# Optimization experiments

Hardware: AMD Instinct MI355X
Metric: run time of the kernel (lower is better)

The kernel has to match this reference:

```python
import jax, jax.numpy as jnp
import numpy as np

B, LQ, LK = 8, 256, 256
Q_SIZE = K_SIZE = H = D_V = 256
MASK_VALUE = -1000000.0


def setup_inputs() -> dict:
    key = jax.random.key(0)
    kq, kk, kv, kl, kwq, kwk, kwv = jax.random.split(key, 7)
    # Linear weights, torch nn.Linear stores (out, in); init ~ U(-1/sqrt(in), 1/sqrt(in))
    def lin(k, out_f, in_f):
        bound = 1.0 / np.sqrt(in_f)
        return jax.random.uniform(k, (out_f, in_f), jnp.float32, -bound, bound)
    return {
        "queries": jax.random.normal(kq, (B, LQ, Q_SIZE), jnp.float32),
        "keyes": jax.random.normal(kk, (B, LK, K_SIZE), jnp.float32),
        "values": jax.random.normal(kv, (B, LK, D_V), jnp.float32),
        "valid_lens": jax.random.randint(kl, (B,), 1, LK + 1),
        "W_q": lin(kwq, H, Q_SIZE),
        "W_k": lin(kwk, H, K_SIZE),
        "W_v": lin(kwv, 1, H),
    }


def reference(queries, keyes, values, valid_lens, W_q, W_k, W_v):
    # Projections (nn.Linear without bias): x @ W.T
    q = jnp.einsum("bqd,hd->bqh", queries, W_q)            # (B, Lq, H)
    k = jnp.einsum("bkd,hd->bkh", keyes, W_k)              # (B, Lk, H)
    # Broadcast-add + tanh: (B, Lq, Lk, H)
    features = jnp.tanh(q[:, :, None, :] + k[:, None, :, :])
    # W_v reduction H -> 1, squeeze: scores (B, Lq, Lk)
    scores = jnp.einsum("bqkh,h->bqk", features, W_v[0])
    # sequence_mask over the last (key) axis with value -1e6
    lk = scores.shape[-1]
    mask = jnp.arange(lk)[None, None, :] < valid_lens[:, None, None]  # (B,1,Lk)
    scores = jnp.where(mask, scores, MASK_VALUE)
    # NOTE: this repo's masked_softmax normalizes over dim=1 (the query axis),
    # faithfully reproduced here.
    attention_weights = jax.nn.softmax(scores, axis=1)
    # dropout is identity in eval / p=0.0
    return jnp.einsum("bqk,bkd->bqd", attention_weights, values)
```

## Files before the change

### kernel.cpp

```cpp
#include <hip/hip_runtime.h>

typedef float vf4 __attribute__((ext_vector_type(4)));

#define MASKV (-1000000.0f)
#define LOG2E 1.4426950408889634f
#define TWO_LOG2E 2.8853900817779268f

__device__ __forceinline__ float fexp2(float x) {
#if __has_builtin(__builtin_amdgcn_exp2f)
  return __builtin_amdgcn_exp2f(x);
#else
  return exp2f(x);
#endif
}
__device__ __forceinline__ float frcp(float x) {
#if __has_builtin(__builtin_amdgcn_rcpf)
  return __builtin_amdgcn_rcpf(x);
#else
  return 1.0f / x;
#endif
}

__global__ __launch_bounds__(256) void proj_kernel(
    const float* __restrict__ queries, const float* __restrict__ keyes,
    const float* __restrict__ Wq, const float* __restrict__ Wk,
    float* __restrict__ Qp, float* __restrict__ Kp) {
  __shared__ alignas(16) float At[16 * 68];
  __shared__ alignas(16) float Bt[16 * 68];
  const int t = threadIdx.x;
  const int m0 = blockIdx.x * 64;
  const int n0 = blockIdx.y * 64;
  const bool isQ = (m0 < 2048);
  const float* X = isQ ? queries : keyes;
  const float* W = isQ ? Wq : Wk;
  float* C = isQ ? Qp : Kp;
  const int mb = isQ ? m0 : (m0 - 2048);

  const int lm = t >> 2;
  const int lq = t & 3;
  const int mm4 = (t & 15) * 4;
  const int nn4 = (t >> 4) * 4;

  float acc[4][4] = {};
  for (int kc = 0; kc < 256; kc += 16) {
    __syncthreads();
    vf4 xa = *(const vf4*)&X[(mb + lm) * 256 + kc + lq * 4];
    vf4 wb = *(const vf4*)&W[(n0 + lm) * 256 + kc + lq * 4];
#pragma unroll
    for (int c = 0; c < 4; ++c) {
      At[(lq * 4 + c) * 68 + lm] = xa[c];
      Bt[(lq * 4 + c) * 68 + lm] = wb[c];
    }
    __syncthreads();
#pragma unroll
    for (int kk = 0; kk < 16; ++kk) {
      vf4 a4 = *(const vf4*)&At[kk * 68 + mm4];
      vf4 b4 = *(const vf4*)&Bt[kk * 68 + nn4];
#pragma unroll
      for (int i = 0; i < 4; ++i)
#pragma unroll
        for (int j = 0; j < 4; ++j) acc[i][j] += a4[i] * b4[j];
    }
  }
#pragma unroll
  for (int i = 0; i < 4; ++i) {
    vf4 o = {acc[i][0] * TWO_LOG2E, acc[i][1] * TWO_LOG2E,
             acc[i][2] * TWO_LOG2E, acc[i][3] * TWO_LOG2E};
    *(vf4*)&C[(mb + mm4 + i) * 256 + n0 + nn4] = o;
  }
}

__global__ __launch_bounds__(256) void scores_kernel(
    const float* __restrict__ Qp, const float* __restrict__ Kp,
    const float* __restrict__ Wv, const int* __restrict__ valid_lens,
    float* __restrict__ ST) {
  __shared__ alignas(16) float Qc[32 * 36];
  __shared__ alignas(16) float Kc[32 * 36];
  __shared__ alignas(16) float wvs[256];
  const int t = threadIdx.x;
  const int b = blockIdx.z;
  const int i0 = blockIdx.x * 32;
  const int j0 = blockIdx.y * 32;

  if (t < 64) *(vf4*)&wvs[t * 4] = *(const vf4*)&Wv[t * 4];
  __syncthreads();

  float Swv;
  {
    vf4 w4 = *(const vf4*)&wvs[(t & 63) * 4];
    float sw = w4[0] + w4[1] + w4[2] + w4[3];
#pragma unroll
    for (int off = 1; off < 64; off <<= 1) sw += __shfl_xor(sw, off, 64);
    Swv = sw;
  }

  const int lr = t >> 3, lq = t & 7;
  const int ti = t & 15, tj = t >> 4;
  float acc[2][2] = {};

  for (int hc = 0; hc < 8; ++hc) {
    __syncthreads();
    vf4 qv = *(const vf4*)&Qp[((b << 8) + i0 + lr) * 256 + hc * 32 + lq * 4];
    vf4 kv = *(const vf4*)&Kp[((b << 8) + j0 + lr) * 256 + hc * 32 + lq * 4];
    *(vf4*)&Qc[lr * 36 + lq * 4] = qv;
    *(vf4*)&Kc[lr * 36 + lq * 4] = kv;
    __syncthreads();
#pragma unroll
    for (int hh = 0; hh < 8; ++hh) {
      vf4 q0 = *(const vf4*)&Qc[ti * 36 + hh * 4];
      vf4 q1 = *(const vf4*)&Qc[(ti + 16) * 36 + hh * 4];
      vf4 k0 = *(const vf4*)&Kc[tj * 36 + hh * 4];
      vf4 k1 = *(const vf4*)&Kc[(tj + 16) * 36 + hh * 4];
      vf4 wv4 = *(const vf4*)&wvs[hc * 32 + hh * 4];
#pragma unroll
      for (int c = 0; c < 4; ++c) {
        acc[0][0] += wv4[c] * frcp(fexp2(q0[c] + k0[c]) + 1.0f);
        acc[0][1] += wv4[c] * frcp(fexp2(q0[c] + k1[c]) + 1.0f);
        acc[1][0] += wv4[c] * frcp(fexp2(q1[c] + k0[c]) + 1.0f);
        acc[1][1] += wv4[c] * frcp(fexp2(q1[c] + k1[c]) + 1.0f);
      }
    }
  }
  const int len = valid_lens[b];
#pragma unroll
  for (int jq = 0; jq < 2; ++jq) {
    const int jg = j0 + tj + jq * 16;
    const bool masked = (jg >= len);
#pragma unroll
    for (int iq = 0; iq < 2; ++iq) {
      const int ig = i0 + ti + iq * 16;
      float s = masked ? MASKV : (Swv - 2.0f * acc[iq][jq]);
      ST[(((b << 8) + jg) << 8) + ig] = s;
    }
  }
}

__global__ __launch_bounds__(256) void softmax_kernel(float* __restrict__ ST) {
  const int t = threadIdx.x;
  const int l = t & 63;
  const int row = blockIdx.x * 4 + (t >> 6);
  vf4* rp = (vf4*)(ST + row * 256);
  vf4 v = rp[l];
  float mx = fmaxf(fmaxf(v[0], v[1]), fmaxf(v[2], v[3]));
#pragma unroll
  for (int off = 1; off < 64; off <<= 1) mx = fmaxf(mx, __shfl_xor(mx, off, 64));
  vf4 e;
#pragma unroll
  for (int c = 0; c < 4; ++c) e[c] = fexp2((v[c] - mx) * LOG2E);
  float s = e[0] + e[1] + e[2] + e[3];
#pragma unroll
  for (int off = 1; off < 64; off <<= 1) s += __shfl_xor(s, off, 64);
  const float r = frcp(s);
#pragma unroll
  for (int c = 0; c < 4; ++c) e[c] *= r;
  rp[l] = e;
}

__global__ __launch_bounds__(256) void out_kernel(
    const float* __restrict__ WT, const float* __restrict__ V,
    float* __restrict__ out) {
  __shared__ alignas(16) float Ws[32 * 36];
  __shared__ alignas(16) float Vs[32 * 36];
  const int t = threadIdx.x;
  const int b = blockIdx.z;
  const int i0 = blockIdx.x * 32;
  const int d0 = blockIdx.y * 32;
  const int jj = t >> 3, lq = t & 7;
  const int ii = t >> 3, dd = (t & 7) * 4;
  vf4 acc = {0.f, 0.f, 0.f, 0.f};
  for (int jc = 0; jc < 8; ++jc) {
    __syncthreads();
    const int jg = jc * 32 + jj;
    *(vf4*)&Ws[jj * 36 + lq * 4] = *(const vf4*)&WT[((b << 8) + jg) * 256 + i0 + lq * 4];
    *(vf4*)&Vs[jj * 36 + lq * 4] = *(const vf4*)&V[((b << 8) + jg) * 256 + d0 + lq * 4];
    __syncthreads();
#pragma unroll
    for (int j2 = 0; j2 < 32; ++j2) {
      const float w = Ws[j2 * 36 + ii];
      vf4 v4 = *(const vf4*)&Vs[j2 * 36 + dd];
      acc += w * v4;
    }
  }
  *(vf4*)&out[((b << 8) + i0 + ii) * 256 + d0 + dd] = acc;
}

extern "C" void kernel_launch(void* const* d_in, const int* in_sizes, int n_in,
                              void* d_out, int out_size, void* d_ws, size_t ws_size,
                              hipStream_t stream) {
  const float* queries = (const float*)d_in[0];
  const float* keyes = (const float*)d_in[1];
  const float* values = (const float*)d_in[2];
  const int* valid_lens = (const int*)d_in[3];
  const float* Wq = (const float*)d_in[4];
  const float* Wk = (const float*)d_in[5];
  const float* Wv = (const float*)d_in[6];
  float* out = (float*)d_out;

  float* Qp = (float*)d_ws;
  float* Kp = Qp + 524288;
  float* ST = Kp + 524288;

  proj_kernel<<<dim3(64, 4, 1), 256, 0, stream>>>(queries, keyes, Wq, Wk, Qp, Kp);
  scores_kernel<<<dim3(8, 8, 8), 256, 0, stream>>>(Qp, Kp, Wv, valid_lens, ST);
  softmax_kernel<<<512, 256, 0, stream>>>(ST);
  out_kernel<<<dim3(8, 8, 8), 256, 0, stream>>>(ST, values, out);
}
```

Baseline: 126.9 us.

## Fuse softmax into scores kernel and retile output GEMM

The scores kernel now has each block compute all 256 query rows for 8 key columns, so the softmax over the query axis runs in registers via wave shuffles before the weights are written. This removes the separate softmax kernel and one read-write pass over the score matrix. The grid shrinks from 512 to 256 blocks, and each block stages a 256x33 Q tile in shared memory, which may reduce occupancy and latency hiding for the tanh-heavy inner loop. The output GEMM is retiled to 128 threads computing 4x4 register tiles over 32x64 output blocks.

```diff
diff --git a/kernel.cpp b/kernel.cpp
--- a/kernel.cpp
+++ b/kernel.cpp
@@ -6,20 +6,8 @@
 #define LOG2E 1.4426950408889634f
 #define TWO_LOG2E 2.8853900817779268f
 
-__device__ __forceinline__ float fexp2(float x) {
-#if __has_builtin(__builtin_amdgcn_exp2f)
-  return __builtin_amdgcn_exp2f(x);
-#else
-  return exp2f(x);
-#endif
-}
-__device__ __forceinline__ float frcp(float x) {
-#if __has_builtin(__builtin_amdgcn_rcpf)
-  return __builtin_amdgcn_rcpf(x);
-#else
-  return 1.0f / x;
-#endif
-}
+__device__ __forceinline__ float fexp2(float x) { return __builtin_amdgcn_exp2f(x); }
+__device__ __forceinline__ float frcp(float x) { return __builtin_amdgcn_rcpf(x); }
 
 __global__ __launch_bounds__(256) void proj_kernel(
     const float* __restrict__ queries, const float* __restrict__ keyes,
@@ -70,118 +58,148 @@
   }
 }
 
-__global__ __launch_bounds__(256) void scores_kernel(
+__global__ __launch_bounds__(256) void scores_softmax_kernel(
     const float* __restrict__ Qp, const float* __restrict__ Kp,
     const float* __restrict__ Wv, const int* __restrict__ valid_lens,
-    float* __restrict__ ST) {
-  __shared__ alignas(16) float Qc[32 * 36];
-  __shared__ alignas(16) float Kc[32 * 36];
+    float* __restrict__ WT) {
+  __shared__ float Qs[256 * 33 + 8];
+  __shared__ float Ks[8 * 33];
   __shared__ alignas(16) float wvs[256];
+  const int t = threadIdx.x;
+  const int b = blockIdx.y;
+  const int j0 = blockIdx.x * 8;
+  const int ti = t & 63;
+  const int tj = t >> 6;
+
+  if (t < 64) *(vf4*)&wvs[t * 4] = *(const vf4*)&Wv[t * 4];
+  __syncthreads();
+
+  float Swv;
+  {
+    vf4 w4 = *(const vf4*)&wvs[ti * 4];
+    float sw = w4[0] + w4[1] + w4[2] + w4[3];
+#pragma unroll
+    for (int off = 1; off < 64; off <<= 1) sw += __shfl_xor(sw, off, 64);
+    Swv = sw;
+  }
+
+  float acc0[4] = {0.f, 0.f, 0.f, 0.f};
+  float acc1[4] = {0.f, 0.f, 0.f, 0.f};
+  const int qr = t >> 2;
+  const int qc = (t & 3) * 8;
+
+  for (int hc = 0; hc < 8; ++hc) {
+    __syncthreads();
+#pragma unroll
+    for (int s = 0; s < 4; ++s) {
+      const int i = s * 64 + qr;
+      const float* src = &Qp[((b << 8) + i) * 256 + hc * 32 + qc];
+      vf4 a = *(const vf4*)src;
+      vf4 bb = *(const vf4*)(src + 4);
+      float* q = &Qs[i * 33 + qc];
+      q[0] = a[0]; q[1] = a[1]; q[2] = a[2]; q[3] = a[3];
+      q[4] = bb[0]; q[5] = bb[1]; q[6] = bb[2]; q[7] = bb[3];
+    }
+    if (t < 64) {
+      const int jj = t >> 3, c = (t & 7) * 4;
+      vf4 kv = *(const vf4*)&Kp[((b << 8) + j0 + jj) * 256 + hc * 32 + c];
+      float* kd = &Ks[jj * 33 + c];
+      kd[0] = kv[0]; kd[1] = kv[1]; kd[2] = kv[2]; kd[3] = kv[3];
+    }
+    __syncthreads();
+#pragma unroll
+    for (int hh = 0; hh < 8; ++hh) {
+      vf4 wv4 = *(const vf4*)&wvs[hc * 32 + hh * 4];
+      float k0[4], k1[4];
+#pragma unroll
+      for (int c = 0; c < 4; ++c) {
+        k0[c] = Ks[(tj * 2 + 0) * 33 + hh * 4 + c];
+        k1[c] = Ks[(tj * 2 + 1) * 33 + hh * 4 + c];
+      }
+#pragma unroll
+      for (int r = 0; r < 4; ++r) {
+        const float* qp = &Qs[(ti + 64 * r) * 33 + hh * 4];
+#pragma unroll
+        for (int c = 0; c < 4; ++c) {
+          const float qv = qp[c];
+          acc0[r] += wv4[c] * frcp(fexp2(qv + k0[c]) + 1.0f);
+          acc1[r] += wv4[c] * frcp(fexp2(qv + k1[c]) + 1.0f);
+        }
+      }
+    }
+  }
+
+  const int len = valid_lens[b];
+#pragma unroll
+  for (int jj = 0; jj < 2; ++jj) {
+    const int j = j0 + tj * 2 + jj;
+    const bool masked = (j >= len);
+    float sc[4];
+#pragma unroll
+    for (int r = 0; r < 4; ++r) {
+      const float a = (jj == 0) ? acc0[r] : acc1[r];
+      sc[r] = masked ? MASKV : (Swv - 2.0f * a);
+    }
+    float m = fmaxf(fmaxf(sc[0], sc[1]), fmaxf(sc[2], sc[3]));
+#pragma unroll
+    for (int off = 1; off < 64; off <<= 1) m = fmaxf(m, __shfl_xor(m, off, 64));
+    float e[4], es = 0.f;
+#pragma unroll
+    for (int r = 0; r < 4; ++r) { e[r] = fexp2((sc[r] - m) * LOG2E); es += e[r]; }
+#pragma unroll
+    for (int off = 1; off < 64; off <<= 1) es += __shfl_xor(es, off, 64);
+    const float rr = frcp(es);
+    float* dst = &WT[((b << 8) + j) << 8];
+#pragma unroll
+    for (int r = 0; r < 4; ++r) dst[ti + 64 * r] = e[r] * rr;
+  }
+}
+
+__global__ __launch_bounds__(128) void out_kernel(
+    const float* __restrict__ WT, const float* __restrict__ V,
+    float* __restrict__ out) {
+  __shared__ alignas(16) float As[32 * 36];
+  __shared__ alignas(16) float Bs[32 * 68];
   const int t = threadIdx.x;
   const int b = blockIdx.z;
   const int i0 = blockIdx.x * 32;
-  const int j0 = blockIdx.y * 32;
-
-  if (t < 64) *(vf4*)&wvs[t * 4] = *(const vf4*)&Wv[t * 4];
-  __syncthreads();
-
-  float Swv;
-  {
-    vf4 w4 = *(const vf4*)&wvs[(t & 63) * 4];
-    float sw = w4[0] + w4[1] + w4[2] + w4[3];
-#pragma unroll
-    for (int off = 1; off < 64; off <<= 1) sw += __shfl_xor(sw, off, 64);
-    Swv = sw;
-  }
-
-  const int lr = t >> 3, lq = t & 7;
-  const int ti = t & 15, tj = t >> 4;
-  float acc[2][2] = {};
-
-  for (int hc = 0; hc < 8; ++hc) {
-    __syncthreads();
-    vf4 qv = *(const vf4*)&Qp[((b << 8) + i0 + lr) * 256 + hc * 32 + lq * 4];
-    vf4 kv = *(const vf4*)&Kp[((b << 8) + j0 + lr) * 256 + hc * 32 + lq * 4];
-    *(vf4*)&Qc[lr * 36 + lq * 4] = qv;
-    *(vf4*)&Kc[lr * 36 + lq * 4] = kv;
-    __syncthreads();
-#pragma unroll
-    for (int hh = 0; hh < 8; ++hh) {
-      vf4 q0 = *(const vf4*)&Qc[ti * 36 + hh * 4];
-      vf4 q1 = *(const vf4*)&Qc[(ti + 16) * 36 + hh * 4];
-      vf4 k0 = *(const vf4*)&Kc[tj * 36 + hh * 4];
-      vf4 k1 = *(const vf4*)&Kc[(tj + 16) * 36 + hh * 4];
-      vf4 wv4 = *(const vf4*)&wvs[hc * 32 + hh * 4];
-#pragma unroll
-      for (int c = 0; c < 4; ++c) {
-        acc[0][0] += wv4[c] * frcp(fexp2(q0[c] + k0[c]) + 1.0f);
-        acc[0][1] += wv4[c] * frcp(fexp2(q0[c] + k1[c]) + 1.0f);
-        acc[1][0] += wv4[c] * frcp(fexp2(q1[c] + k0[c]) + 1.0f);
-        acc[1][1] += wv4[c] * frcp(fexp2(q1[c] + k1[c]) + 1.0f);
-      }
-    }
-  }
-  const int len = valid_lens[b];
-#pragma unroll
-  for (int jq = 0; jq < 2; ++jq) {
-    const int jg = j0 + tj + jq * 16;
-    const bool masked = (jg >= len);
-#pragma unroll
-    for (int iq = 0; iq < 2; ++iq) {
-      const int ig = i0 + ti + iq * 16;
-      float s = masked ? MASKV : (Swv - 2.0f * acc[iq][jq]);
-      ST[(((b << 8) + jg) << 8) + ig] = s;
-    }
-  }
-}
-
-__global__ __launch_bounds__(256) void softmax_kernel(float* __restrict__ ST) {
-  const int t = threadIdx.x;
-  const int l = t & 63;
-  const int row = blockIdx.x * 4 + (t >> 6);
-  vf4* rp = (vf4*)(ST + row * 256);
-  vf4 v = rp[l];
-  float mx = fmaxf(fmaxf(v[0], v[1]), fmaxf(v[2], v[3]));
-#pragma unroll
-  for (int off = 1; off < 64; off <<= 1) mx = fmaxf(mx, __shfl_xor(mx, off, 64));
-  vf4 e;
-#pragma unroll
-  for (int c = 0; c < 4; ++c) e[c] = fexp2((v[c] - mx) * LOG2E);
-  float s = e[0] + e[1] + e[2] + e[3];
-#pragma unroll
-  for (int off = 1; off < 64; off <<= 1) s += __shfl_xor(s, off, 64);
-  const float r = frcp(s);
-#pragma unroll
-  for (int c = 0; c < 4; ++c) e[c] *= r;
-  rp[l] = e;
-}
-
-__global__ __launch_bounds__(256) void out_kernel(
-    const float* __restrict__ WT, const float* __restrict__ V,
-    float* __restrict__ out) {
-  __shared__ alignas(16) float Ws[32 * 36];
-  __shared__ alignas(16) float Vs[32 * 36];
-  const int t = threadIdx.x;
-  const int b = blockIdx.z;
-  const int i0 = blockIdx.x * 32;
-  const int d0 = blockIdx.y * 32;
-  const int jj = t >> 3, lq = t & 7;
-  const int ii = t >> 3, dd = (t & 7) * 4;
-  vf4 acc = {0.f, 0.f, 0.f, 0.f};
+  const int d0 = blockIdx.y * 64;
+  const int tm = t & 7;
+  const int tn = t >> 3;
+  const int sr = t >> 2;
+  const int sc4 = (t & 3) * 4;
+  float acc[4][4] = {};
   for (int jc = 0; jc < 8; ++jc) {
     __syncthreads();
-    const int jg = jc * 32 + jj;
-    *(vf4*)&Ws[jj * 36 + lq * 4] = *(const vf4*)&WT[((b << 8) + jg) * 256 + i0 + lq * 4];
-    *(vf4*)&Vs[jj * 36 + lq * 4] = *(const vf4*)&V[((b << 8) + jg) * 256 + d0 + lq * 4];
-    __syncthreads();
-#pragma unroll
-    for (int j2 = 0; j2 < 32; ++j2) {
-      const float w = Ws[j2 * 36 + ii];
-      vf4 v4 = *(const vf4*)&Vs[j2 * 36 + dd];
-      acc += w * v4;
-    }
-  }
-  *(vf4*)&out[((b << 8) + i0 + ii) * 256 + d0 + dd] = acc;
+    const int jbase = jc * 32;
+#pragma unroll
+    for (int s = 0; s < 2; ++s) {
+      const int col = sc4 + s * 16;
+      *(vf4*)&As[sr * 36 + col] =
+          *(const vf4*)&WT[((b << 8) + jbase + sr) * 256 + i0 + col];
+    }
+#pragma unroll
+    for (int s = 0; s < 4; ++s) {
+      const int col = sc4 + s * 16;
+      *(vf4*)&Bs[sr * 68 + col] =
+          *(const vf4*)&V[((b << 8) + jbase + sr) * 256 + d0 + col];
+    }
+    __syncthreads();
+#pragma unroll
+    for (int kk = 0; kk < 32; ++kk) {
+      vf4 a4 = *(const vf4*)&As[kk * 36 + tm * 4];
+      vf4 b4 = *(const vf4*)&Bs[kk * 68 + tn * 4];
+#pragma unroll
+      for (int i = 0; i < 4; ++i)
+#pragma unroll
+        for (int j = 0; j < 4; ++j) acc[i][j] += a4[i] * b4[j];
+    }
+  }
+#pragma unroll
+  for (int i = 0; i < 4; ++i) {
+    vf4 o = {acc[i][0], acc[i][1], acc[i][2], acc[i][3]};
+    *(vf4*)&out[((b << 8) + i0 + tm * 4 + i) * 256 + d0 + tn * 4] = o;
+  }
 }
 
 extern "C" void kernel_launch(void* const* d_in, const int* in_sizes, int n_in,
@@ -198,10 +216,9 @@
 
   float* Qp = (float*)d_ws;
   float* Kp = Qp + 524288;
-  float* ST = Kp + 524288;
-
-  proj_kernel<<<dim3(64, 4, 1), 256, 0, stream>>>(queries, keyes, Wq, Wk, Qp, Kp);
-  scores_kernel<<<dim3(8, 8, 8), 256, 0, stream>>>(Qp, Kp, Wv, valid_lens, ST);
-  softmax_kernel<<<512, 256, 0, stream>>>(ST);
-  out_kernel<<<dim3(8, 8, 8), 256, 0, stream>>>(ST, values, out);
-}
+  float* WT = Kp + 524288;
+
+  proj_kernel<<<dim3(64, 4), 256, 0, stream>>>(queries, keyes, Wq, Wk, Qp, Kp);
+  scores_softmax_kernel<<<dim3(32, 8), 256, 0, stream>>>(Qp, Kp, Wv, valid_lens, WT);
+  out_kernel<<<dim3(8, 4, 8), 128, 0, stream>>>(WT, values, out);
+}
```

After: 136.5 us. 7.6% more time.

## Fold softmax exp into scores kernel and apply normalization inside output GEMM

Applied to the files above, without the earlier changes.

The scores kernel now writes exp(score) directly, with no max subtraction, since the scores are bounded by the sum of |W_v|. Masked keys get 1.0, which still gives a uniform softmax across the query axis. A light rowsum kernel stores reciprocal sums, and the output GEMM scales E by them as it loads tiles. This removes the separate softmax read-modify-write pass. The scores kernel also gets an XOR-swizzled LDS layout, and the output kernel is retiled to 4x4 per thread with 128-thread blocks. The risk is that skipping max subtraction could overflow exp if score magnitudes were larger than W_v bounds them to.

```diff
diff --git a/kernel.cpp b/kernel.cpp
--- a/kernel.cpp
+++ b/kernel.cpp
@@ -2,24 +2,11 @@
 
 typedef float vf4 __attribute__((ext_vector_type(4)));
 
-#define MASKV (-1000000.0f)
 #define LOG2E 1.4426950408889634f
 #define TWO_LOG2E 2.8853900817779268f
 
-__device__ __forceinline__ float fexp2(float x) {
-#if __has_builtin(__builtin_amdgcn_exp2f)
-  return __builtin_amdgcn_exp2f(x);
-#else
-  return exp2f(x);
-#endif
-}
-__device__ __forceinline__ float frcp(float x) {
-#if __has_builtin(__builtin_amdgcn_rcpf)
-  return __builtin_amdgcn_rcpf(x);
-#else
-  return 1.0f / x;
-#endif
-}
+__device__ __forceinline__ float fexp2(float x) { return __builtin_amdgcn_exp2f(x); }
+__device__ __forceinline__ float frcp(float x) { return __builtin_amdgcn_rcpf(x); }
 
 __global__ __launch_bounds__(256) void proj_kernel(
     const float* __restrict__ queries, const float* __restrict__ keyes,
@@ -70,118 +57,136 @@
   }
 }
 
-__global__ __launch_bounds__(256) void scores_kernel(
+__global__ __launch_bounds__(256) void scores_exp_kernel(
     const float* __restrict__ Qp, const float* __restrict__ Kp,
     const float* __restrict__ Wv, const int* __restrict__ valid_lens,
-    float* __restrict__ ST) {
-  __shared__ alignas(16) float Qc[32 * 36];
-  __shared__ alignas(16) float Kc[32 * 36];
+    float* __restrict__ E) {
+  __shared__ alignas(16) float Qs[32 * 32];
+  __shared__ alignas(16) float Ks[32 * 32];
   __shared__ alignas(16) float wvs[256];
   const int t = threadIdx.x;
-  const int b = blockIdx.z;
   const int i0 = blockIdx.x * 32;
   const int j0 = blockIdx.y * 32;
-
-  if (t < 64) *(vf4*)&wvs[t * 4] = *(const vf4*)&Wv[t * 4];
-  __syncthreads();
+  const int b = blockIdx.z;
+  const int ti = t & 15;
+  const int tj = t >> 4;
 
   float Swv;
   {
-    vf4 w4 = *(const vf4*)&wvs[(t & 63) * 4];
+    vf4 w4 = *(const vf4*)&Wv[(t & 63) * 4];
     float sw = w4[0] + w4[1] + w4[2] + w4[3];
 #pragma unroll
     for (int off = 1; off < 64; off <<= 1) sw += __shfl_xor(sw, off, 64);
     Swv = sw;
   }
-
-  const int lr = t >> 3, lq = t & 7;
-  const int ti = t & 15, tj = t >> 4;
+  if (t < 64) *(vf4*)&wvs[t * 4] = *(const vf4*)&Wv[t * 4];
+
+  const int srow = t >> 3;
+  const int scg = t & 7;
+  const int swcol = ((scg ^ (srow & 7)) << 2);
+  const int qxor = ti & 7;
+  const int kxor = tj & 7;
+
   float acc[2][2] = {};
-
   for (int hc = 0; hc < 8; ++hc) {
     __syncthreads();
-    vf4 qv = *(const vf4*)&Qp[((b << 8) + i0 + lr) * 256 + hc * 32 + lq * 4];
-    vf4 kv = *(const vf4*)&Kp[((b << 8) + j0 + lr) * 256 + hc * 32 + lq * 4];
-    *(vf4*)&Qc[lr * 36 + lq * 4] = qv;
-    *(vf4*)&Kc[lr * 36 + lq * 4] = kv;
+    vf4 qv = *(const vf4*)&Qp[(((b << 8) + i0 + srow) << 8) + hc * 32 + scg * 4];
+    vf4 kv = *(const vf4*)&Kp[(((b << 8) + j0 + srow) << 8) + hc * 32 + scg * 4];
+    *(vf4*)&Qs[srow * 32 + swcol] = qv;
+    *(vf4*)&Ks[srow * 32 + swcol] = kv;
     __syncthreads();
 #pragma unroll
     for (int hh = 0; hh < 8; ++hh) {
-      vf4 q0 = *(const vf4*)&Qc[ti * 36 + hh * 4];
-      vf4 q1 = *(const vf4*)&Qc[(ti + 16) * 36 + hh * 4];
-      vf4 k0 = *(const vf4*)&Kc[tj * 36 + hh * 4];
-      vf4 k1 = *(const vf4*)&Kc[(tj + 16) * 36 + hh * 4];
+      vf4 q0 = *(const vf4*)&Qs[ti * 32 + ((hh ^ qxor) << 2)];
+      vf4 q1 = *(const vf4*)&Qs[(ti + 16) * 32 + ((hh ^ qxor) << 2)];
+      vf4 k0 = *(const vf4*)&Ks[tj * 32 + ((hh ^ kxor) << 2)];
+      vf4 k1 = *(const vf4*)&Ks[(tj + 16) * 32 + ((hh ^ kxor) << 2)];
       vf4 wv4 = *(const vf4*)&wvs[hc * 32 + hh * 4];
 #pragma unroll
-      for (int c = 0; c < 4; ++c) {
-        acc[0][0] += wv4[c] * frcp(fexp2(q0[c] + k0[c]) + 1.0f);
-        acc[0][1] += wv4[c] * frcp(fexp2(q0[c] + k1[c]) + 1.0f);
-        acc[1][0] += wv4[c] * frcp(fexp2(q1[c] + k0[c]) + 1.0f);
-        acc[1][1] += wv4[c] * frcp(fexp2(q1[c] + k1[c]) + 1.0f);
+      for (int e = 0; e < 4; ++e) {
+        const float we = wv4[e];
+        acc[0][0] += we * frcp(fexp2(q0[e] + k0[e]) + 1.0f);
+        acc[0][1] += we * frcp(fexp2(q0[e] + k1[e]) + 1.0f);
+        acc[1][0] += we * frcp(fexp2(q1[e] + k0[e]) + 1.0f);
+        acc[1][1] += we * frcp(fexp2(q1[e] + k1[e]) + 1.0f);
       }
     }
   }
+
   const int len = valid_lens[b];
 #pragma unroll
-  for (int jq = 0; jq < 2; ++jq) {
-    const int jg = j0 + tj + jq * 16;
-    const bool masked = (jg >= len);
-#pragma unroll
-    for (int iq = 0; iq < 2; ++iq) {
-      const int ig = i0 + ti + iq * 16;
-      float s = masked ? MASKV : (Swv - 2.0f * acc[iq][jq]);
-      ST[(((b << 8) + jg) << 8) + ig] = s;
-    }
-  }
-}
-
-__global__ __launch_bounds__(256) void softmax_kernel(float* __restrict__ ST) {
+  for (int c = 0; c < 2; ++c) {
+    const int j = j0 + tj + 16 * c;
+    const bool masked = (j >= len);
+#pragma unroll
+    for (int r = 0; r < 2; ++r) {
+      const int i = i0 + ti + 16 * r;
+      const float score = Swv - 2.0f * acc[r][c];
+      const float ev = masked ? 1.0f : fexp2(score * LOG2E);
+      E[(((b << 8) + j) << 8) + i] = ev;
+    }
+  }
+}
+
+__global__ __launch_bounds__(256) void rowsum_kernel(
+    const float* __restrict__ E, float* __restrict__ R) {
   const int t = threadIdx.x;
   const int l = t & 63;
   const int row = blockIdx.x * 4 + (t >> 6);
-  vf4* rp = (vf4*)(ST + row * 256);
-  vf4 v = rp[l];
-  float mx = fmaxf(fmaxf(v[0], v[1]), fmaxf(v[2], v[3]));
-#pragma unroll
-  for (int off = 1; off < 64; off <<= 1) mx = fmaxf(mx, __shfl_xor(mx, off, 64));
-  vf4 e;
-#pragma unroll
-  for (int c = 0; c < 4; ++c) e[c] = fexp2((v[c] - mx) * LOG2E);
-  float s = e[0] + e[1] + e[2] + e[3];
+  vf4 v = *(const vf4*)&E[(row << 8) + l * 4];
+  float s = v[0] + v[1] + v[2] + v[3];
 #pragma unroll
   for (int off = 1; off < 64; off <<= 1) s += __shfl_xor(s, off, 64);
-  const float r = frcp(s);
-#pragma unroll
-  for (int c = 0; c < 4; ++c) e[c] *= r;
-  rp[l] = e;
-}
-
-__global__ __launch_bounds__(256) void out_kernel(
-    const float* __restrict__ WT, const float* __restrict__ V,
-    float* __restrict__ out) {
-  __shared__ alignas(16) float Ws[32 * 36];
-  __shared__ alignas(16) float Vs[32 * 36];
-  const int t = threadIdx.x;
+  if (l == 0) R[row] = frcp(s);
+}
+
+__global__ __launch_bounds__(128) void out_kernel(
+    const float* __restrict__ E, const float* __restrict__ R,
+    const float* __restrict__ V, float* __restrict__ out) {
+  __shared__ alignas(16) float As[32 * 36];
+  __shared__ alignas(16) float Bs[32 * 68];
+  const int t = threadIdx.x;
+  const int i0 = blockIdx.x * 32;
+  const int d0 = blockIdx.y * 64;
   const int b = blockIdx.z;
-  const int i0 = blockIdx.x * 32;
-  const int d0 = blockIdx.y * 32;
-  const int jj = t >> 3, lq = t & 7;
-  const int ii = t >> 3, dd = (t & 7) * 4;
-  vf4 acc = {0.f, 0.f, 0.f, 0.f};
+  const int ti = t & 7;
+  const int td = t >> 3;
+  const int srow = t >> 2;
+  const int scg = t & 3;
+
+  float acc[4][4] = {};
   for (int jc = 0; jc < 8; ++jc) {
-    __syncthreads();
-    const int jg = jc * 32 + jj;
-    *(vf4*)&Ws[jj * 36 + lq * 4] = *(const vf4*)&WT[((b << 8) + jg) * 256 + i0 + lq * 4];
-    *(vf4*)&Vs[jj * 36 + lq * 4] = *(const vf4*)&V[((b << 8) + jg) * 256 + d0 + lq * 4];
-    __syncthreads();
-#pragma unroll
-    for (int j2 = 0; j2 < 32; ++j2) {
-      const float w = Ws[j2 * 36 + ii];
-      vf4 v4 = *(const vf4*)&Vs[j2 * 36 + dd];
-      acc += w * v4;
-    }
-  }
-  *(vf4*)&out[((b << 8) + i0 + ii) * 256 + d0 + dd] = acc;
+    const int jb = jc * 32;
+    __syncthreads();
+    const float rj = R[(b << 8) + jb + srow];
+#pragma unroll
+    for (int s = 0; s < 2; ++s) {
+      const int col = scg * 8 + s * 4;
+      vf4 a = *(const vf4*)&E[(((b << 8) + jb + srow) << 8) + i0 + col];
+      *(vf4*)&As[srow * 36 + col] = a * rj;
+    }
+#pragma unroll
+    for (int s = 0; s < 4; ++s) {
+      const int col = scg * 16 + s * 4;
+      *(vf4*)&Bs[srow * 68 + col] =
+          *(const vf4*)&V[(((b << 8) + jb + srow) << 8) + d0 + col];
+    }
+    __syncthreads();
+#pragma unroll
+    for (int j = 0; j < 32; ++j) {
+      vf4 a4 = *(const vf4*)&As[j * 36 + ti * 4];
+      vf4 b4 = *(const vf4*)&Bs[j * 68 + td * 4];
+#pragma unroll
+      for (int r = 0; r < 4; ++r)
+#pragma unroll
+        for (int c = 0; c < 4; ++c) acc[r][c] += a4[r] * b4[c];
+    }
+  }
+#pragma unroll
+  for (int r = 0; r < 4; ++r) {
+    vf4 o = {acc[r][0], acc[r][1], acc[r][2], acc[r][3]};
+    *(vf4*)&out[(((b << 8) + i0 + ti * 4 + r) << 8) + d0 + td * 4] = o;
+  }
 }
 
 extern "C" void kernel_launch(void* const* d_in, const int* in_sizes, int n_in,
@@ -198,10 +203,11 @@
 
   float* Qp = (float*)d_ws;
   float* Kp = Qp + 524288;
-  float* ST = Kp + 524288;
-
-  proj_kernel<<<dim3(64, 4, 1), 256, 0, stream>>>(queries, keyes, Wq, Wk, Qp, Kp);
-  scores_kernel<<<dim3(8, 8, 8), 256, 0, stream>>>(Qp, Kp, Wv, valid_lens, ST);
-  softmax_kernel<<<512, 256, 0, stream>>>(ST);
-  out_kernel<<<dim3(8, 8, 8), 256, 0, stream>>>(ST, values, out);
-}
+  float* E = Kp + 524288;
+  float* R = E + 524288;
+
+  proj_kernel<<<dim3(64, 4), 256, 0, stream>>>(queries, keyes, Wq, Wk, Qp, Kp);
+  scores_exp_kernel<<<dim3(8, 8, 8), 256, 0, stream>>>(Qp, Kp, Wv, valid_lens, E);
+  rowsum_kernel<<<512, 256, 0, stream>>>(E, R);
+  out_kernel<<<dim3(8, 4, 8), 128, 0, stream>>>(E, R, values, out);
+}
```

New measurement: 129.7 us. 2.2% more time.
